# Performance work log

Hardware: AMD Instinct MI355X
Metric: run time of the kernel (lower is better)

## Reference

```python
import jax, jax.numpy as jnp
import numpy as np

N_NODES = 20000
D = 8


def setup_inputs() -> dict:
    key = jax.random.key(0)
    k1, k2, k3 = jax.random.split(key, 3)
    E_half = 250000
    src = jax.random.randint(k1, (E_half,), 0, N_NODES, dtype=jnp.int32)
    dst = jax.random.randint(k2, (E_half,), 0, N_NODES, dtype=jnp.int32)
    # builder expects both edge directions present (symmetric edge set)
    row = jnp.concatenate([src, dst])
    col = jnp.concatenate([dst, src])
    edge_index = jnp.stack([row, col])  # (2, 500000) int32
    E = row.shape[0]
    restriction_maps = jax.random.normal(k3, (E, D, D), dtype=jnp.float32)
    return {"restriction_maps": restriction_maps, "edge_index": edge_index}


def _sheaf_adjacency_values(restriction_maps, edge_index, n=N_NODES):
    """Faithful port of SheafAdjacencyBuilder: transport maps + sparse values
    with self-loops and symmetric normalization. Returns the normalized sparse
    value vector of length (E + n) * d * d (off-diagonal blocks then diagonal)."""
    row, col = edge_index[0], edge_index[1]
    E = row.shape[0]
    d = restriction_maps.shape[-1]
    # --- reverse-edge lookup via hashed searchsorted (matches torch source) ---
    eh = row * n + col              # fits int32 for n=20000
    rh = col * n + row
    order = jnp.argsort(eh)
    sorted_h = eh[order]
    pos = jnp.clip(jnp.searchsorted(sorted_h, rh), 0, E - 1)
    rev = jnp.where(sorted_h[pos] == rh, order[pos], jnp.arange(E, dtype=order.dtype))
    # --- per-edge transport maps P_ij = F_src^T @ F_dst, shape (E, d, d) ---
    P = jnp.einsum('eji,ejk->eik', restriction_maps, restriction_maps[rev])
    # --- sparse block indices ---
    dr = jnp.arange(d, dtype=jnp.int32)
    off_row = jnp.broadcast_to(row[:, None, None] * d + dr[None, :, None], (E, d, d)).reshape(-1)
    off_col = jnp.broadcast_to(col[:, None, None] * d + dr[None, None, :], (E, d, d)).reshape(-1)
    node_base = jnp.arange(n, dtype=jnp.int32) * d
    diag_row = jnp.broadcast_to(node_base[:, None, None] + dr[None, :, None], (n, d, d)).reshape(-1)
    diag_col = jnp.broadcast_to(node_base[:, None, None] + dr[None, None, :], (n, d, d)).reshape(-1)
    eye_vals = jnp.broadcast_to(jnp.eye(d, dtype=restriction_maps.dtype), (n, d, d)).reshape(-1)
    rows = jnp.concatenate([off_row, diag_row])
    cols = jnp.concatenate([off_col, diag_col])
    vals = jnp.concatenate([P.reshape(-1), eye_vals])
    # --- symmetric normalization D^{-1/2} A D^{-1/2} (deg of |values|) ---
    Nd = n * d
    deg = jax.ops.segment_sum(jnp.abs(vals), rows, num_segments=Nd)
    deg_safe = jnp.where(deg > 0, deg, 1.0)
    dinv = jnp.where(deg > 0, deg_safe ** -0.5, 0.0)
    return dinv[rows] * vals * dinv[cols]


def reference(restriction_maps, edge_index):
    return _sheaf_adjacency_values(restriction_maps, edge_index)
```

## Files before the change

### kernel.cpp

```cpp
#include <hip/hip_runtime.h>
#include <stdint.h>

constexpr int NN   = 20000;
constexpr int DD   = 8;
constexpr int ND   = NN * DD;
constexpr uint32_t HSIZE = 1u << 20;
constexpr uint32_t HMASK = HSIZE - 1;
constexpr unsigned long long EMPTY64 = ~0ULL;

typedef float v4f __attribute__((ext_vector_type(4)));

__device__ __forceinline__ uint32_t hkey(uint32_t k) {
    k *= 2654435761u;
    return k ^ (k >> 15);
}

__global__ void k_fill(unsigned long long* __restrict__ slots,
                       float* __restrict__ deg) {
    uint32_t i = blockIdx.x * blockDim.x + threadIdx.x;
    if (i < HSIZE / 2) {
        ulonglong2 v; v.x = EMPTY64; v.y = EMPTY64;
        ((ulonglong2*)slots)[i] = v;
    }
    if (i < (uint32_t)ND) deg[i] = 1.0f;
}

__global__ void k_insert(const int* __restrict__ row, const int* __restrict__ col,
                         unsigned long long* __restrict__ slots, int E) {
    int e = blockIdx.x * blockDim.x + threadIdx.x;
    if (e >= E) return;
    uint32_t key = (uint32_t)(row[e] * NN + col[e]);
    unsigned long long cur = ((unsigned long long)key << 19) | (unsigned)e;
    uint32_t s = hkey(key) & HMASK;
    while (true) {
        unsigned long long old = atomicMin(&slots[s], cur);
        if (old == EMPTY64) break;
        if ((uint32_t)(old >> 19) == key) break;
        if (old > cur) { cur = old; key = (uint32_t)(cur >> 19); }
        s = (s + 1) & HMASK;
    }
}

__global__ void k_revcls(const int* __restrict__ row, const int* __restrict__ col,
                         const unsigned long long* __restrict__ slots,
                         int* __restrict__ task, int E) {
    int e = blockIdx.x * blockDim.x + threadIdx.x;
    if (e >= E) return;
    int r = row[e], c = col[e];
    uint32_t kf = (uint32_t)(r * NN + c);
    uint32_t kr = (uint32_t)(c * NN + r);
    uint32_t sf = hkey(kf) & HMASK;
    uint32_t sr = hkey(kr) & HMASK;
    int f = e, me = e;
    bool dr_ = false, dm_ = false;
    while (true) {
        unsigned long long vr, vm;
        if (!dr_) vr = slots[sr];
        if (!dm_) vm = slots[sf];
        if (!dr_) {
            if (vr == EMPTY64) dr_ = true;
            else if ((uint32_t)(vr >> 19) == kr) { f = (int)(vr & 0x7FFFFu); dr_ = true; }
            else sr = (sr + 1) & HMASK;
        }
        if (!dm_) {
            if (vm == EMPTY64) dm_ = true;
            else if ((uint32_t)(vm >> 19) == kf) { me = (int)(vm & 0x7FFFFu); dm_ = true; }
            else sf = (sf + 1) & HMASK;
        }
        if (dr_ && dm_) break;
    }
    int cls = (f == e) ? 1 : ((me == e) ? ((e < f) ? 2 : 0) : 1);
    task[e] = f | (cls << 29);
}

__global__ void __launch_bounds__(256)
k_deg(const float* __restrict__ F,
      const int* __restrict__ row, const int* __restrict__ col,
      const int* __restrict__ task, float* __restrict__ deg, int E) {
    __shared__ float fa[32 * 68];
    __shared__ float fb[32 * 68];
    __shared__ int s_f[32], s_cls[32], s_row[32], s_col[32];
    const int t  = threadIdx.x;
    const int e0 = blockIdx.x * 32;

    if (t < 32) {
        int e = e0 + t;
        int cls = 0, f = 0;
        if (e < E) {
            int w = task[e];
            cls = w >> 29;
            f   = w & ((1 << 29) - 1);
            s_row[t] = row[e];
            s_col[t] = col[e];
        }
        s_cls[t] = cls;
        s_f[t]   = f;
    }
    __syncthreads();

    const float4* F4 = (const float4*)F;
    #pragma unroll
    for (int p = 0; p < 2; ++p) {
        int q = t + p * 256, es = q >> 4, sub = q & 15, off = sub << 2;
        int ge = e0 + es;
        if (ge < E && s_cls[es]) {
            *(float4*)&fa[es * 68 + off] = F4[(size_t)ge * 16 + sub];
            *(float4*)&fb[es * 68 + off] = F4[(size_t)s_f[es] * 16 + sub];
        }
    }
    __syncthreads();

    const int es = t >> 3, i = t & 7, e = e0 + es;
    if (e >= E) return;
    const int cls = s_cls[es];
    if (!cls) return;

    const float* fav = &fa[es * 68];
    const float* fbv = &fb[es * 68];
    float acc0 = 0.f, acc1 = 0.f, acc2 = 0.f, acc3 = 0.f;
    float acc4 = 0.f, acc5 = 0.f, acc6 = 0.f, acc7 = 0.f;
    #pragma unroll
    for (int j = 0; j < 8; ++j) {
        float  a  = fav[j * 8 + i];
        float4 b0 = *(const float4*)&fbv[j * 8];
        float4 b1 = *(const float4*)&fbv[j * 8 + 4];
        acc0 = fmaf(a, b0.x, acc0);  acc1 = fmaf(a, b0.y, acc1);
        acc2 = fmaf(a, b0.z, acc2);  acc3 = fmaf(a, b0.w, acc3);
        acc4 = fmaf(a, b1.x, acc4);  acc5 = fmaf(a, b1.y, acc5);
        acc6 = fmaf(a, b1.z, acc6);  acc7 = fmaf(a, b1.w, acc7);
    }
    float b0 = fabsf(acc0), b1 = fabsf(acc1), b2 = fabsf(acc2), b3 = fabsf(acc3);
    float b4 = fabsf(acc4), b5 = fabsf(acc5), b6 = fabsf(acc6), b7 = fabsf(acc7);
    float rs = b0 + b1 + b2 + b3 + b4 + b5 + b6 + b7;
    atomicAdd(&deg[s_row[es] * DD + i], rs);

    if (cls == 2) {
        #pragma unroll
        for (int m = 1; m < 8; m <<= 1) {
            b0 += __shfl_xor(b0, m);  b1 += __shfl_xor(b1, m);
            b2 += __shfl_xor(b2, m);  b3 += __shfl_xor(b3, m);
            b4 += __shfl_xor(b4, m);  b5 += __shfl_xor(b5, m);
            b6 += __shfl_xor(b6, m);  b7 += __shfl_xor(b7, m);
        }
        float ci = (i & 4) ? ((i & 2) ? ((i & 1) ? b7 : b6) : ((i & 1) ? b5 : b4))
                           : ((i & 2) ? ((i & 1) ? b3 : b2) : ((i & 1) ? b1 : b0));
        atomicAdd(&deg[s_col[es] * DD + i], ci);
    }
}

__global__ void k_dinv_diag(const float* __restrict__ deg, float* __restrict__ dinv,
                            float* __restrict__ out, int E) {
    int r = blockIdx.x * blockDim.x + threadIdx.x;
    if (r >= ND) return;
    float dv = 1.0f / sqrtf(deg[r]);
    dinv[r] = dv;
    float dd = dv * dv;
    int i = r & 7;
    v4f a = { 0.f, 0.f, 0.f, 0.f };
    v4f b = { 0.f, 0.f, 0.f, 0.f };
    if (i < 4) a[i] = dd; else b[i - 4] = dd;
    size_t base = (size_t)E * 64 + (size_t)(r >> 3) * 64 + (size_t)i * 8;
    __builtin_nontemporal_store(a, (v4f*)&out[base]);
    __builtin_nontemporal_store(b, (v4f*)&out[base + 4]);
}

__global__ void __launch_bounds__(256)
k_pnorm(const float* __restrict__ F,
        const int* __restrict__ row, const int* __restrict__ col,
        const int* __restrict__ task, const float* __restrict__ dinv,
        float* __restrict__ out, int E) {
    __shared__ float fa[32 * 68];
    __shared__ float fb[32 * 68];
    __shared__ int s_f[32], s_cls[32], s_row[32], s_col[32];
    const int t  = threadIdx.x;
    const int e0 = blockIdx.x * 32;

    if (t < 32) {
        int e = e0 + t;
        int cls = 0, f = 0;
        if (e < E) {
            int w = task[e];
            cls = w >> 29;
            f   = w & ((1 << 29) - 1);
            s_row[t] = row[e];
            s_col[t] = col[e];
        }
        s_cls[t] = cls;
        s_f[t]   = f;
    }
    __syncthreads();

    const float4* F4 = (const float4*)F;
    #pragma unroll
    for (int p = 0; p < 2; ++p) {
        int q = t + p * 256, es = q >> 4, sub = q & 15, off = sub << 2;
        int ge = e0 + es;
        if (ge < E && s_cls[es]) {
            *(float4*)&fa[es * 68 + off] = F4[(size_t)ge * 16 + sub];
            *(float4*)&fb[es * 68 + off] = F4[(size_t)s_f[es] * 16 + sub];
        }
    }
    __syncthreads();

    const int es = t >> 3, i = t & 7, e = e0 + es;
    if (e >= E) return;
    const int cls = s_cls[es];
    if (!cls) return;

    const float* fav = &fa[es * 68];
    const float* fbv = &fb[es * 68];
    float acc0 = 0.f, acc1 = 0.f, acc2 = 0.f, acc3 = 0.f;
    float acc4 = 0.f, acc5 = 0.f, acc6 = 0.f, acc7 = 0.f;
    #pragma unroll
    for (int j = 0; j < 8; ++j) {
        float  a  = fav[j * 8 + i];
        float4 b0 = *(const float4*)&fbv[j * 8];
        float4 b1 = *(const float4*)&fbv[j * 8 + 4];
        acc0 = fmaf(a, b0.x, acc0);  acc1 = fmaf(a, b0.y, acc1);
        acc2 = fmaf(a, b0.z, acc2);  acc3 = fmaf(a, b0.w, acc3);
        acc4 = fmaf(a, b1.x, acc4);  acc5 = fmaf(a, b1.y, acc5);
        acc6 = fmaf(a, b1.z, acc6);  acc7 = fmaf(a, b1.w, acc7);
    }

    const int r = s_row[es], c = s_col[es];
    float dr  = dinv[r * DD + i];
    v4f  dc0  = *(const v4f*)&dinv[c * DD];
    v4f  dc1  = *(const v4f*)&dinv[c * DD + 4];

    float v[8];
    v[0] = acc0 * dr * dc0.x;  v[1] = acc1 * dr * dc0.y;
    v[2] = acc2 * dr * dc0.z;  v[3] = acc3 * dr * dc0.w;
    v[4] = acc4 * dr * dc1.x;  v[5] = acc5 * dr * dc1.y;
    v[6] = acc6 * dr * dc1.z;  v[7] = acc7 * dr * dc1.w;

    v4f w0 = { v[0], v[1], v[2], v[3] };
    v4f w1 = { v[4], v[5], v[6], v[7] };
    size_t ob = (size_t)e * 64 + i * 8;
    __builtin_nontemporal_store(w0, (v4f*)&out[ob]);
    __builtin_nontemporal_store(w1, (v4f*)&out[ob + 4]);

    if (cls == 2) {
        #pragma unroll
        for (int m = 1; m < 8; m <<= 1) {
            #pragma unroll
            for (int j = 0; j < 8; ++j) {
                if ((j & m) == 0) {
                    float sel = (i & m) ? v[j] : v[j | m];
                    float got = __shfl_xor(sel, m);
                    float nj  = (i & m) ? got : v[j];
                    float njm = (i & m) ? v[j | m] : got;
                    v[j] = nj;  v[j | m] = njm;
                }
            }
        }
        v4f u0 = { v[0], v[1], v[2], v[3] };
        v4f u1 = { v[4], v[5], v[6], v[7] };
        size_t fb_ = (size_t)s_f[es] * 64 + i * 8;
        __builtin_nontemporal_store(u0, (v4f*)&out[fb_]);
        __builtin_nontemporal_store(u1, (v4f*)&out[fb_ + 4]);
    }
}

extern "C" void kernel_launch(void* const* d_in, const int* in_sizes, int n_in,
                              void* d_out, int out_size, void* d_ws, size_t ws_size,
                              hipStream_t stream) {
    const float* F  = (const float*)d_in[0];
    const int*   ei = (const int*)d_in[1];
    const int E = in_sizes[1] / 2;
    const int* row = ei;
    const int* col = ei + E;

    unsigned long long* slots = (unsigned long long*)d_ws;
    int*   task = (int*)(slots + HSIZE);
    float* deg  = (float*)(task + E);
    float* dinv = deg + ND;
    float* out  = (float*)d_out;

    k_fill     <<<(HSIZE / 2 + 255) / 256, 256, 0, stream>>>(slots, deg);
    k_insert   <<<(E + 255) / 256,   256, 0, stream>>>(row, col, slots, E);
    k_revcls   <<<(E + 255) / 256,   256, 0, stream>>>(row, col, slots, task, E);
    k_deg      <<<(E + 31) / 32,     256, 0, stream>>>(F, row, col, task, deg, E);
    k_dinv_diag<<<(ND + 255) / 256,  256, 0, stream>>>(deg, dinv, out, E);
    k_pnorm    <<<(E + 31) / 32,     256, 0, stream>>>(F, row, col, task, dinv, out, E);
}
```

Baseline: 158.7 us.

## Fuse reverse-edge lookup into degree kernel and pair edges e and e+E/2 per block

Removes the separate reverse-lookup kernel by doing the hash probes inside the degree kernel. Each block now handles edge e together with e+E/2, which is usually its reverse edge given the symmetric layout, so a reverse map already in shared memory can be reused instead of fetched again. When the pair does not match, the kernel falls back to a hash probe and a direct global read of the partner map. This relies on the input's half-and-half layout for the reuse to pay off but stays correct for any input, at the cost of more divergent per-thread probing inside the heavier kernel.

```diff
diff --git a/kernel.cpp b/kernel.cpp
--- a/kernel.cpp
+++ b/kernel.cpp
@@ -13,6 +13,32 @@
 __device__ __forceinline__ uint32_t hkey(uint32_t k) {
     k *= 2654435761u;
     return k ^ (k >> 15);
+}
+
+__device__ __forceinline__ int hprobe(const unsigned long long* __restrict__ slots,
+                                      uint32_t key, int fallback) {
+    uint32_t s = hkey(key) & HMASK;
+    while (true) {
+        unsigned long long v = slots[s];
+        if (v == EMPTY64) return fallback;
+        if ((uint32_t)(v >> 19) == key) return (int)(v & 0x7FFFFu);
+        s = (s + 1) & HMASK;
+    }
+}
+
+__device__ __forceinline__ void mac8(const float* __restrict__ fav,
+                                     const float* __restrict__ fbv,
+                                     int i, float* __restrict__ acc) {
+#pragma unroll
+    for (int j = 0; j < 8; ++j) {
+        float  a  = fav[j * 8 + i];
+        float4 b0 = *(const float4*)&fbv[j * 8];
+        float4 b1 = *(const float4*)&fbv[j * 8 + 4];
+        acc[0] = fmaf(a, b0.x, acc[0]);  acc[1] = fmaf(a, b0.y, acc[1]);
+        acc[2] = fmaf(a, b0.z, acc[2]);  acc[3] = fmaf(a, b0.w, acc[3]);
+        acc[4] = fmaf(a, b1.x, acc[4]);  acc[5] = fmaf(a, b1.y, acc[5]);
+        acc[6] = fmaf(a, b1.z, acc[6]);  acc[7] = fmaf(a, b1.w, acc[7]);
+    }
 }
 
 __global__ void k_fill(unsigned long long* __restrict__ slots,
@@ -41,110 +67,84 @@
     }
 }
 
-__global__ void k_revcls(const int* __restrict__ row, const int* __restrict__ col,
-                         const unsigned long long* __restrict__ slots,
-                         int* __restrict__ task, int E) {
-    int e = blockIdx.x * blockDim.x + threadIdx.x;
-    if (e >= E) return;
-    int r = row[e], c = col[e];
-    uint32_t kf = (uint32_t)(r * NN + c);
-    uint32_t kr = (uint32_t)(c * NN + r);
-    uint32_t sf = hkey(kf) & HMASK;
-    uint32_t sr = hkey(kr) & HMASK;
-    int f = e, me = e;
-    bool dr_ = false, dm_ = false;
-    while (true) {
-        unsigned long long vr, vm;
-        if (!dr_) vr = slots[sr];
-        if (!dm_) vm = slots[sf];
-        if (!dr_) {
-            if (vr == EMPTY64) dr_ = true;
-            else if ((uint32_t)(vr >> 19) == kr) { f = (int)(vr & 0x7FFFFu); dr_ = true; }
-            else sr = (sr + 1) & HMASK;
-        }
-        if (!dm_) {
-            if (vm == EMPTY64) dm_ = true;
-            else if ((uint32_t)(vm >> 19) == kf) { me = (int)(vm & 0x7FFFFu); dm_ = true; }
-            else sf = (sf + 1) & HMASK;
-        }
-        if (dr_ && dm_) break;
-    }
-    int cls = (f == e) ? 1 : ((me == e) ? ((e < f) ? 2 : 0) : 1);
-    task[e] = f | (cls << 29);
-}
-
 __global__ void __launch_bounds__(256)
 k_deg(const float* __restrict__ F,
       const int* __restrict__ row, const int* __restrict__ col,
-      const int* __restrict__ task, float* __restrict__ deg, int E) {
-    __shared__ float fa[32 * 68];
-    __shared__ float fb[32 * 68];
-    __shared__ int s_f[32], s_cls[32], s_row[32], s_col[32];
+      const unsigned long long* __restrict__ slots, int* __restrict__ task,
+      float* __restrict__ deg, int E, int EH) {
+    __shared__ float fa[64 * 68];
+    __shared__ int s_x[64], s_me[64], s_f[64], s_cls[64], s_row[64], s_col[64];
     const int t  = threadIdx.x;
-    const int e0 = blockIdx.x * 32;
-
-    if (t < 32) {
-        int e = e0 + t;
+    const int b0 = blockIdx.x * 32;
+
+    if (t < 64) {
+        int s = t;
+        int x = (s < 32) ? (b0 + s) : (EH + b0 + (s - 32));
+        bool valid = (s < 32) ? (x < EH) : (x < E);
+        int r = 0, c = 0, me = -1;
+        if (valid) {
+            r = row[x]; c = col[x];
+            me = hprobe(slots, (uint32_t)(r * NN + c), x);
+        } else x = -1;
+        s_x[s] = x; s_row[s] = r; s_col[s] = c; s_me[s] = me;
+    }
+    __syncthreads();
+
+    if (t < 64) {
+        int s = t, x = s_x[s];
         int cls = 0, f = 0;
-        if (e < E) {
-            int w = task[e];
-            cls = w >> 29;
-            f   = w & ((1 << 29) - 1);
-            s_row[t] = row[e];
-            s_col[t] = col[e];
+        if (x >= 0) {
+            int q = s ^ 32;
+            int r = s_row[s], c = s_col[s], me = s_me[s];
+            if (s_x[q] >= 0 && s_row[q] == c && s_col[q] == r) f = s_me[q];
+            else f = hprobe(slots, (uint32_t)(c * NN + r), x);
+            cls = (f == x) ? 1 : ((me == x) ? ((x < f) ? 2 : 0) : 1);
+            task[x] = f | (cls << 29);
         }
-        s_cls[t] = cls;
-        s_f[t]   = f;
-    }
-    __syncthreads();
+        s_f[s] = f; s_cls[s] = cls;
+    }
 
     const float4* F4 = (const float4*)F;
-    #pragma unroll
-    for (int p = 0; p < 2; ++p) {
-        int q = t + p * 256, es = q >> 4, sub = q & 15, off = sub << 2;
-        int ge = e0 + es;
-        if (ge < E && s_cls[es]) {
-            *(float4*)&fa[es * 68 + off] = F4[(size_t)ge * 16 + sub];
-            *(float4*)&fb[es * 68 + off] = F4[(size_t)s_f[es] * 16 + sub];
+#pragma unroll
+    for (int p = 0; p < 4; ++p) {
+        int q = t + p * 256;
+        int sl = q >> 4, sub = q & 15;
+        int x = s_x[sl];
+        if (x >= 0)
+            *(float4*)&fa[sl * 68 + (sub << 2)] = F4[(size_t)x * 16 + sub];
+    }
+    __syncthreads();
+
+    const int g = t >> 3, i = t & 7;
+#pragma unroll
+    for (int item = 0; item < 2; ++item) {
+        int s = (item == 0) ? g : (g + 32);
+        int q = s ^ 32;
+        int x = s_x[s];
+        int cls = (x >= 0) ? s_cls[s] : 0;
+        if (cls) {
+            int f = s_f[s];
+            const float* fav = &fa[s * 68];
+            float acc[8] = {0,0,0,0,0,0,0,0};
+            const float* lsrc = (f == s_x[q]) ? &fa[q * 68] : ((f == x) ? fav : nullptr);
+            if (lsrc) mac8(fav, lsrc, i, acc);
+            else      mac8(fav, F + (size_t)f * 64, i, acc);
+            float b0=fabsf(acc[0]),b1=fabsf(acc[1]),b2=fabsf(acc[2]),b3=fabsf(acc[3]);
+            float b4=fabsf(acc[4]),b5=fabsf(acc[5]),b6=fabsf(acc[6]),b7=fabsf(acc[7]);
+            atomicAdd(&deg[s_row[s] * DD + i], b0+b1+b2+b3+b4+b5+b6+b7);
+            if (cls == 2) {
+#pragma unroll
+                for (int m = 1; m < 8; m <<= 1) {
+                    b0+=__shfl_xor(b0,m); b1+=__shfl_xor(b1,m);
+                    b2+=__shfl_xor(b2,m); b3+=__shfl_xor(b3,m);
+                    b4+=__shfl_xor(b4,m); b5+=__shfl_xor(b5,m);
+                    b6+=__shfl_xor(b6,m); b7+=__shfl_xor(b7,m);
+                }
+                float ci = (i&4) ? ((i&2)?((i&1)?b7:b6):((i&1)?b5:b4))
+                                 : ((i&2)?((i&1)?b3:b2):((i&1)?b1:b0));
+                atomicAdd(&deg[s_col[s] * DD + i], ci);
+            }
         }
-    }
-    __syncthreads();
-
-    const int es = t >> 3, i = t & 7, e = e0 + es;
-    if (e >= E) return;
-    const int cls = s_cls[es];
-    if (!cls) return;
-
-    const float* fav = &fa[es * 68];
-    const float* fbv = &fb[es * 68];
-    float acc0 = 0.f, acc1 = 0.f, acc2 = 0.f, acc3 = 0.f;
-    float acc4 = 0.f, acc5 = 0.f, acc6 = 0.f, acc7 = 0.f;
-    #pragma unroll
-    for (int j = 0; j < 8; ++j) {
-        float  a  = fav[j * 8 + i];
-        float4 b0 = *(const float4*)&fbv[j * 8];
-        float4 b1 = *(const float4*)&fbv[j * 8 + 4];
-        acc0 = fmaf(a, b0.x, acc0);  acc1 = fmaf(a, b0.y, acc1);
-        acc2 = fmaf(a, b0.z, acc2);  acc3 = fmaf(a, b0.w, acc3);
-        acc4 = fmaf(a, b1.x, acc4);  acc5 = fmaf(a, b1.y, acc5);
-        acc6 = fmaf(a, b1.z, acc6);  acc7 = fmaf(a, b1.w, acc7);
-    }
-    float b0 = fabsf(acc0), b1 = fabsf(acc1), b2 = fabsf(acc2), b3 = fabsf(acc3);
-    float b4 = fabsf(acc4), b5 = fabsf(acc5), b6 = fabsf(acc6), b7 = fabsf(acc7);
-    float rs = b0 + b1 + b2 + b3 + b4 + b5 + b6 + b7;
-    atomicAdd(&deg[s_row[es] * DD + i], rs);
-
-    if (cls == 2) {
-        #pragma unroll
-        for (int m = 1; m < 8; m <<= 1) {
-            b0 += __shfl_xor(b0, m);  b1 += __shfl_xor(b1, m);
-            b2 += __shfl_xor(b2, m);  b3 += __shfl_xor(b3, m);
-            b4 += __shfl_xor(b4, m);  b5 += __shfl_xor(b5, m);
-            b6 += __shfl_xor(b6, m);  b7 += __shfl_xor(b7, m);
-        }
-        float ci = (i & 4) ? ((i & 2) ? ((i & 1) ? b7 : b6) : ((i & 1) ? b5 : b4))
-                           : ((i & 2) ? ((i & 1) ? b3 : b2) : ((i & 1) ? b1 : b0));
-        atomicAdd(&deg[s_col[es] * DD + i], ci);
     }
 }
 
@@ -168,96 +168,91 @@
 k_pnorm(const float* __restrict__ F,
         const int* __restrict__ row, const int* __restrict__ col,
         const int* __restrict__ task, const float* __restrict__ dinv,
-        float* __restrict__ out, int E) {
-    __shared__ float fa[32 * 68];
-    __shared__ float fb[32 * 68];
-    __shared__ int s_f[32], s_cls[32], s_row[32], s_col[32];
+        float* __restrict__ out, int E, int EH) {
+    __shared__ float fa[64 * 68];
+    __shared__ int s_x[64], s_f[64], s_cls[64], s_row[64], s_col[64];
     const int t  = threadIdx.x;
-    const int e0 = blockIdx.x * 32;
-
-    if (t < 32) {
-        int e = e0 + t;
-        int cls = 0, f = 0;
-        if (e < E) {
-            int w = task[e];
+    const int b0 = blockIdx.x * 32;
+
+    if (t < 64) {
+        int s = t;
+        int x = (s < 32) ? (b0 + s) : (EH + b0 + (s - 32));
+        bool valid = (s < 32) ? (x < EH) : (x < E);
+        int cls = 0, f = 0, r = 0, c = 0;
+        if (valid) {
+            int w = task[x];
             cls = w >> 29;
             f   = w & ((1 << 29) - 1);
-            s_row[t] = row[e];
-            s_col[t] = col[e];
-        }
-        s_cls[t] = cls;
-        s_f[t]   = f;
+            r = row[x]; c = col[x];
+        } else x = -1;
+        s_x[s] = x; s_f[s] = f; s_cls[s] = cls; s_row[s] = r; s_col[s] = c;
     }
     __syncthreads();
 
     const float4* F4 = (const float4*)F;
-    #pragma unroll
-    for (int p = 0; p < 2; ++p) {
-        int q = t + p * 256, es = q >> 4, sub = q & 15, off = sub << 2;
-        int ge = e0 + es;
-        if (ge < E && s_cls[es]) {
-            *(float4*)&fa[es * 68 + off] = F4[(size_t)ge * 16 + sub];
-            *(float4*)&fb[es * 68 + off] = F4[(size_t)s_f[es] * 16 + sub];
-        }
-    }
-    __syncthreads();
-
-    const int es = t >> 3, i = t & 7, e = e0 + es;
-    if (e >= E) return;
-    const int cls = s_cls[es];
-    if (!cls) return;
-
-    const float* fav = &fa[es * 68];
-    const float* fbv = &fb[es * 68];
-    float acc0 = 0.f, acc1 = 0.f, acc2 = 0.f, acc3 = 0.f;
-    float acc4 = 0.f, acc5 = 0.f, acc6 = 0.f, acc7 = 0.f;
-    #pragma unroll
-    for (int j = 0; j < 8; ++j) {
-        float  a  = fav[j * 8 + i];
-        float4 b0 = *(const float4*)&fbv[j * 8];
-        float4 b1 = *(const float4*)&fbv[j * 8 + 4];
-        acc0 = fmaf(a, b0.x, acc0);  acc1 = fmaf(a, b0.y, acc1);
-        acc2 = fmaf(a, b0.z, acc2);  acc3 = fmaf(a, b0.w, acc3);
-        acc4 = fmaf(a, b1.x, acc4);  acc5 = fmaf(a, b1.y, acc5);
-        acc6 = fmaf(a, b1.z, acc6);  acc7 = fmaf(a, b1.w, acc7);
-    }
-
-    const int r = s_row[es], c = s_col[es];
-    float dr  = dinv[r * DD + i];
-    v4f  dc0  = *(const v4f*)&dinv[c * DD];
-    v4f  dc1  = *(const v4f*)&dinv[c * DD + 4];
-
-    float v[8];
-    v[0] = acc0 * dr * dc0.x;  v[1] = acc1 * dr * dc0.y;
-    v[2] = acc2 * dr * dc0.z;  v[3] = acc3 * dr * dc0.w;
-    v[4] = acc4 * dr * dc1.x;  v[5] = acc5 * dr * dc1.y;
-    v[6] = acc6 * dr * dc1.z;  v[7] = acc7 * dr * dc1.w;
-
-    v4f w0 = { v[0], v[1], v[2], v[3] };
-    v4f w1 = { v[4], v[5], v[6], v[7] };
-    size_t ob = (size_t)e * 64 + i * 8;
-    __builtin_nontemporal_store(w0, (v4f*)&out[ob]);
-    __builtin_nontemporal_store(w1, (v4f*)&out[ob + 4]);
-
-    if (cls == 2) {
-        #pragma unroll
-        for (int m = 1; m < 8; m <<= 1) {
-            #pragma unroll
-            for (int j = 0; j < 8; ++j) {
-                if ((j & m) == 0) {
-                    float sel = (i & m) ? v[j] : v[j | m];
-                    float got = __shfl_xor(sel, m);
-                    float nj  = (i & m) ? got : v[j];
-                    float njm = (i & m) ? v[j | m] : got;
-                    v[j] = nj;  v[j | m] = njm;
+#pragma unroll
+    for (int p = 0; p < 4; ++p) {
+        int q = t + p * 256;
+        int sl = q >> 4, sub = q & 15;
+        int x = s_x[sl];
+        if (x >= 0)
+            *(float4*)&fa[sl * 68 + (sub << 2)] = F4[(size_t)x * 16 + sub];
+    }
+    __syncthreads();
+
+    const int g = t >> 3, i = t & 7;
+#pragma unroll
+    for (int item = 0; item < 2; ++item) {
+        int s = (item == 0) ? g : (g + 32);
+        int q = s ^ 32;
+        int x = s_x[s];
+        int cls = (x >= 0) ? s_cls[s] : 0;
+        if (cls) {
+            int f = s_f[s];
+            const float* fav = &fa[s * 68];
+            float acc[8] = {0,0,0,0,0,0,0,0};
+            const float* lsrc = (f == s_x[q]) ? &fa[q * 68] : ((f == x) ? fav : nullptr);
+            if (lsrc) mac8(fav, lsrc, i, acc);
+            else      mac8(fav, F + (size_t)f * 64, i, acc);
+
+            const int r = s_row[s], c = s_col[s];
+            float dr = dinv[r * DD + i];
+            v4f dc0 = *(const v4f*)&dinv[c * DD];
+            v4f dc1 = *(const v4f*)&dinv[c * DD + 4];
+
+            float v[8];
+            v[0]=acc[0]*dr*dc0.x; v[1]=acc[1]*dr*dc0.y;
+            v[2]=acc[2]*dr*dc0.z; v[3]=acc[3]*dr*dc0.w;
+            v[4]=acc[4]*dr*dc1.x; v[5]=acc[5]*dr*dc1.y;
+            v[6]=acc[6]*dr*dc1.z; v[7]=acc[7]*dr*dc1.w;
+
+            v4f w0 = { v[0], v[1], v[2], v[3] };
+            v4f w1 = { v[4], v[5], v[6], v[7] };
+            size_t ob = (size_t)x * 64 + i * 8;
+            __builtin_nontemporal_store(w0, (v4f*)&out[ob]);
+            __builtin_nontemporal_store(w1, (v4f*)&out[ob + 4]);
+
+            if (cls == 2) {
+#pragma unroll
+                for (int m = 1; m < 8; m <<= 1) {
+#pragma unroll
+                    for (int j = 0; j < 8; ++j) {
+                        if ((j & m) == 0) {
+                            float sel = (i & m) ? v[j] : v[j | m];
+                            float got = __shfl_xor(sel, m);
+                            float nj  = (i & m) ? got : v[j];
+                            float njm = (i & m) ? v[j | m] : got;
+                            v[j] = nj;  v[j | m] = njm;
+                        }
+                    }
                 }
+                v4f u0 = { v[0], v[1], v[2], v[3] };
+                v4f u1 = { v[4], v[5], v[6], v[7] };
+                size_t fb_ = (size_t)f * 64 + i * 8;
+                __builtin_nontemporal_store(u0, (v4f*)&out[fb_]);
+                __builtin_nontemporal_store(u1, (v4f*)&out[fb_ + 4]);
             }
         }
-        v4f u0 = { v[0], v[1], v[2], v[3] };
-        v4f u1 = { v[4], v[5], v[6], v[7] };
-        size_t fb_ = (size_t)s_f[es] * 64 + i * 8;
-        __builtin_nontemporal_store(u0, (v4f*)&out[fb_]);
-        __builtin_nontemporal_store(u1, (v4f*)&out[fb_ + 4]);
     }
 }
 
@@ -269,6 +264,8 @@
     const int E = in_sizes[1] / 2;
     const int* row = ei;
     const int* col = ei + E;
+    const int EH = E / 2;
+    const int NB = ((E - EH) + 31) / 32;
 
     unsigned long long* slots = (unsigned long long*)d_ws;
     int*   task = (int*)(slots + HSIZE);
@@ -277,9 +274,8 @@
     float* out  = (float*)d_out;
 
     k_fill     <<<(HSIZE / 2 + 255) / 256, 256, 0, stream>>>(slots, deg);
-    k_insert   <<<(E + 255) / 256,   256, 0, stream>>>(row, col, slots, E);
-    k_revcls   <<<(E + 255) / 256,   256, 0, stream>>>(row, col, slots, task, E);
-    k_deg      <<<(E + 31) / 32,     256, 0, stream>>>(F, row, col, task, deg, E);
-    k_dinv_diag<<<(ND + 255) / 256,  256, 0, stream>>>(deg, dinv, out, E);
-    k_pnorm    <<<(E + 31) / 32,     256, 0, stream>>>(F, row, col, task, dinv, out, E);
-}
+    k_insert   <<<(E + 255) / 256,  256, 0, stream>>>(row, col, slots, E);
+    k_deg      <<<NB,               256, 0, stream>>>(F, row, col, slots, task, deg, E, EH);
+    k_dinv_diag<<<(ND + 255) / 256, 256, 0, stream>>>(deg, dinv, out, E);
+    k_pnorm    <<<NB,               256, 0, stream>>>(F, row, col, task, dinv, out, E, EH);
+}
```

Measured after the change: 144.9 us. 1.1x faster.
